# Kernel tuning notes

Measured on AMD Instinct MI355X. Metric: run time of the kernel, lower is better.

The kernel has to match this reference:

```python
import jax, jax.numpy as jnp
import numpy as np

N_NODES = 100000
N_EDGES = 1600000
IN_CH = 128
HID = 128
EMBED = 256
NUM_GRAPHS = 128


def setup_inputs() -> dict:
    key = jax.random.key(0)
    ks = jax.random.split(key, 12)
    x = jax.random.normal(ks[0], (N_NODES, IN_CH), dtype=jnp.float32)
    edge_index = jax.random.randint(ks[1], (2, N_EDGES), 0, N_NODES, dtype=jnp.int64)
    batch = jnp.sort(jax.random.randint(ks[2], (N_NODES,), 0, NUM_GRAPHS, dtype=jnp.int64))
    s = 0.05
    # conv1 MLP: Linear(in_ch,128) -> ReLU -> Linear(128,128)
    W11 = jax.random.normal(ks[3], (IN_CH, HID), dtype=jnp.float32) * s
    b11 = jnp.zeros((HID,), dtype=jnp.float32)
    W12 = jax.random.normal(ks[4], (HID, HID), dtype=jnp.float32) * s
    b12 = jnp.zeros((HID,), dtype=jnp.float32)
    # conv2 MLP: Linear(128,128) -> ReLU -> Linear(128,embed)
    W21 = jax.random.normal(ks[5], (HID, HID), dtype=jnp.float32) * s
    b21 = jnp.zeros((HID,), dtype=jnp.float32)
    W22 = jax.random.normal(ks[6], (HID, EMBED), dtype=jnp.float32) * s
    b22 = jnp.zeros((EMBED,), dtype=jnp.float32)
    gamma = jnp.ones((EMBED,), dtype=jnp.float32)
    beta = jnp.zeros((EMBED,), dtype=jnp.float32)
    return {"x": x, "edge_index": edge_index, "batch": batch,
            "W11": W11, "b11": b11, "W12": W12, "b12": b12,
            "W21": W21, "b21": b21, "W22": W22, "b22": b22,
            "gamma": gamma, "beta": beta}


def _gin_conv(x, src, dst, W_a, b_a, W_b, b_b):
    # GINConv with eps=0: MLP(x + sum_{j in N(i)} x_j)
    msgs = x[src]                                   # [E, d] gather
    agg = jax.ops.segment_sum(msgs, dst, num_segments=N_NODES)  # scatter-add
    h = x + agg
    h = jax.nn.relu(h @ W_a + b_a)
    return h @ W_b + b_b


def reference(x, edge_index, batch, W11, b11, W12, b12, W21, b21, W22, b22, gamma, beta):
    src, dst = edge_index[0], edge_index[1]
    h = jax.nn.relu(_gin_conv(x, src, dst, W11, b11, W12, b12))   # [N, 128]
    h = jax.nn.relu(_gin_conv(h, src, dst, W21, b21, W22, b22))   # [N, 256]
    # global_mean_pool over graphs
    sums = jax.ops.segment_sum(h, batch, num_segments=NUM_GRAPHS)           # [G, 256]
    counts = jax.ops.segment_sum(jnp.ones((N_NODES,), h.dtype), batch, num_segments=NUM_GRAPHS)
    pooled = sums / jnp.maximum(counts, 1.0)[:, None]
    # LayerNorm over last dim (eps=1e-5 as in torch)
    mu = jnp.mean(pooled, axis=-1, keepdims=True)
    var = jnp.var(pooled, axis=-1, keepdims=True)
    out = (pooled - mu) * jax.lax.rsqrt(var + 1e-5) * gamma + beta
    # Dropout in eval mode: identity
    return out
```

## Files before the change

kernel.cpp:

```cpp
#include <hip/hip_runtime.h>

#define GRAPHS 128
#define CHUNKC 4000

typedef _Float16 f16x8 __attribute__((ext_vector_type(8)));
typedef _Float16 f16x4 __attribute__((ext_vector_type(4)));
typedef _Float16 f16x2 __attribute__((ext_vector_type(2)));
typedef float f32x4 __attribute__((ext_vector_type(4)));

__device__ __forceinline__ void fmix_lo(float& a, int w) {
  asm("v_fma_mix_f32 %0, %1, 1.0, %0 op_sel:[0,0,0] op_sel_hi:[1,0,0]" : "+v"(a) : "v"(w));
}
__device__ __forceinline__ void fmix_hi(float& a, int w) {
  asm("v_fma_mix_f32 %0, %1, 1.0, %0 op_sel:[1,0,0] op_sel_hi:[1,0,0]" : "+v"(a) : "v"(w));
}

__global__ void k_hist(const int* __restrict__ dst, int* __restrict__ histG,
                       int e, int NB, int NW) {
  __shared__ int h[256];
  int t = threadIdx.x, w = blockIdx.x;
  h[t] = 0; __syncthreads();
  int lo = w * CHUNKC, hi = min(lo + CHUNKC, e);
  for (int i = lo + t; i < hi; i += 256) atomicAdd(&h[dst[i] >> 9], 1);
  __syncthreads();
  if (t < NB) histG[t * NW + w] = h[t];
}

__global__ void k_scanA(const int* __restrict__ in, int* __restrict__ out,
                        int* __restrict__ bsum, int N) {
  __shared__ int s[256];
  int t = threadIdx.x, b = blockIdx.x;
  int base = b * 1024 + t * 4;
  int v[4]; int tot = 0;
#pragma unroll
  for (int j = 0; j < 4; ++j) { int i = base + j; v[j] = (i < N) ? in[i] : 0; tot += v[j]; }
  s[t] = tot; __syncthreads();
  for (int o = 1; o < 256; o <<= 1) {
    int x = (t >= o) ? s[t - o] : 0;
    __syncthreads(); s[t] += x; __syncthreads();
  }
  int run = s[t] - tot;
#pragma unroll
  for (int j = 0; j < 4; ++j) { int i = base + j; if (i < N) out[i] = run; run += v[j]; }
  if (t == 255) bsum[b] = s[255];
}

__global__ void k_scanB(int* bsum, int nb, const int* __restrict__ batch,
                        int* __restrict__ starts, int n) {
  __shared__ int s[256];
  int t = threadIdx.x;
  int v = (t < nb) ? bsum[t] : 0;
  s[t] = v; __syncthreads();
  for (int o = 1; o < 256; o <<= 1) {
    int x = (t >= o) ? s[t - o] : 0;
    __syncthreads(); s[t] += x; __syncthreads();
  }
  if (t < nb) bsum[t] = s[t] - v;
  if (t <= GRAPHS) {
    int lo = 0, hi = n;
    while (lo < hi) { int mid = (lo + hi) >> 1; if (batch[mid] < t) lo = mid + 1; else hi = mid; }
    starts[t] = lo;
  }
}

__global__ void k_scanC(int* __restrict__ out, const int* __restrict__ bsum, int N) {
  int i = blockIdx.x * 256 + threadIdx.x;
  if (i < N) out[i] += bsum[i >> 10];
}

__global__ void k_part(const int* __restrict__ src, const int* __restrict__ dst,
                       const int* __restrict__ histG, const int* __restrict__ off,
                       int* __restrict__ part, int e, int NB, int NW) {
  __shared__ int hist[256], lbA[256], lbB[256], stmp[256];
  __shared__ int els[CHUNKC];
  int t = threadIdx.x, w = blockIdx.x;
  int hv = (t < NB) ? histG[t * NW + w] : 0;
  hist[t] = hv; stmp[t] = hv; __syncthreads();
  for (int o = 1; o < 256; o <<= 1) {
    int x = (t >= o) ? stmp[t - o] : 0;
    __syncthreads(); stmp[t] += x; __syncthreads();
  }
  lbA[t] = stmp[t] - hv; lbB[t] = stmp[t] - hv;
  __syncthreads();
  int lo = w * CHUNKC, hi = min(lo + CHUNKC, e);
  for (int i = lo + t; i < hi; i += 256) {
    int d = dst[i];
    int p = atomicAdd(&lbB[d >> 9], 1);
    els[p] = src[i] | ((d & 511) << 17);
  }
  __syncthreads();
  int ln = t & 63, wv = t >> 6;
  for (int b = wv; b < NB; b += 4) {
    int c = hist[b], lb = lbA[b];
    long g = off[b * NW + w];
    for (int j = ln; j < c; j += 64) part[g + j] = els[lb + j];
  }
}

__global__ void k_csrb(const int* __restrict__ part, const int* __restrict__ off,
                       int* __restrict__ ptr, int* __restrict__ csr,
                       int e, int NB, int NW, int n) {
  __shared__ int nh[512], ncur[512], stmp[256];
  int t = threadIdx.x, b = blockIdx.x;
  int s0 = off[b * NW];
  int e0 = (b + 1 < NB) ? off[(b + 1) * NW] : e;
  nh[t] = 0; nh[t + 256] = 0; __syncthreads();
  for (int i = s0 + t; i < e0; i += 256) atomicAdd(&nh[((unsigned)part[i]) >> 17], 1);
  __syncthreads();
  int v0 = nh[2 * t], v1 = nh[2 * t + 1];
  int ps = v0 + v1;
  stmp[t] = ps; __syncthreads();
  for (int o = 1; o < 256; o <<= 1) {
    int x = (t >= o) ? stmp[t - o] : 0;
    __syncthreads(); stmp[t] += x; __syncthreads();
  }
  int base = stmp[t] - ps;
  __syncthreads();
  nh[2 * t] = base;   nh[2 * t + 1] = base + v0;
  ncur[2 * t] = base; ncur[2 * t + 1] = base + v0;
  __syncthreads();
#pragma unroll
  for (int q = 0; q < 2; ++q) {
    int vv = t + q * 256;
    int node = (b << 9) + vv;
    if (node <= n) ptr[node] = s0 + nh[vv];
  }
  for (int i = s0 + t; i < e0; i += 256) {
    int u = part[i];
    int p = atomicAdd(&ncur[((unsigned)u) >> 17], 1);
    csr[s0 + p] = u & 0x1FFFF;
  }
}

__global__ void k_prep(const float* __restrict__ x, _Float16* __restrict__ P0,
                       _Float16* __restrict__ P1, int n,
                       const float* __restrict__ W11, const float* __restrict__ W12,
                       const float* __restrict__ W21, const float* __restrict__ W22,
                       f16x8* __restrict__ f11, f16x8* __restrict__ f12,
                       f16x8* __restrict__ f21, f16x8* __restrict__ f22,
                       float* __restrict__ pool, int cvtb, int wpb, int poolb) {
  int b = blockIdx.x, t = threadIdx.x;
  if (b < cvtb) {
    int i = b * 256 + t;
    if (i < n * 32) {
      float4 v = ((const float4*)x)[i];
      f16x4 h = { (_Float16)v.x, (_Float16)v.y, (_Float16)v.z, (_Float16)v.w };
      ((f16x4*)P0)[i] = h;
    }
    return;
  }
  b -= cvtb;
  if (b < wpb) {
    int id = b * 256 + t;
    const float* W; f16x8* F; int C, cid, fshift;
    if (id < 2048)       { W = W11; F = f11; C = 128; cid = id;        fshift = 3; }
    else if (id < 4096)  { W = W12; F = f12; C = 128; cid = id - 2048; fshift = 3; }
    else if (id < 6144)  { W = W21; F = f21; C = 128; cid = id - 4096; fshift = 3; }
    else if (id < 10240) { W = W22; F = f22; C = 256; cid = id - 6144; fshift = 4; }
    else return;
    int lane = cid & 63;
    int rest = cid >> 6;
    int fc = rest & ((1 << fshift) - 1);
    int kk = rest >> fshift;
    int cout = fc * 16 + (lane & 15);
    int kb = kk * 32 + (lane >> 4) * 8;
    f16x8 v;
#pragma unroll
    for (int q = 0; q < 8; ++q) v[q] = (_Float16)W[(size_t)(kb + q) * C + cout];
    F[cid] = v;
    return;
  }
  b -= wpb;
  if (b < poolb) {
    int i = b * 256 + t;
    if (i < GRAPHS * 256) pool[i] = 0.f;
    return;
  }
  if (t < 128) P0[(size_t)n * 128 + t] = (_Float16)0.f;
  else P1[(size_t)n * 128 + (t - 128)] = (_Float16)0.f;
}

__global__ void k_agg_h(const _Float16* __restrict__ in, _Float16* __restrict__ out,
                        const int* __restrict__ ptr, const int* __restrict__ csr, int n) {
  int gid = blockIdx.x * 256 + threadIdx.x;
  int node = gid >> 6, lane = gid & 63;
  if (node >= n) return;
  const f16x8* inp = (const f16x8*)in;
  int cb = lane & 15, rg = lane >> 4;
  f16x8 self = inp[(size_t)node * 16 + cb];
  float acc[8];
#pragma unroll
  for (int c = 0; c < 8; ++c) acc[c] = (rg == 0) ? (float)self[c] : 0.f;
  int s = ptr[node], deg = ptr[node + 1] - s;
  union W { f16x8 v; int i[4]; };
  for (int seg = 0; seg < deg; seg += 64) {
    int my = (seg + lane < deg) ? csr[s + seg + lane] : n;
    int segn = min(deg - seg, 64);
    for (int b2 = 0; b2 < segn; b2 += 32) {
      int jj[8]; W w[8];
#pragma unroll
      for (int u = 0; u < 8; ++u) jj[u] = __shfl(my, b2 + u * 4 + rg);
#pragma unroll
      for (int u = 0; u < 8; ++u) w[u].v = inp[(size_t)jj[u] * 16 + cb];
#pragma unroll
      for (int u = 0; u < 8; ++u)
#pragma unroll
        for (int p = 0; p < 4; ++p) {
          fmix_lo(acc[2 * p], w[u].i[p]);
          fmix_hi(acc[2 * p + 1], w[u].i[p]);
        }
    }
  }
#pragma unroll
  for (int c = 0; c < 8; ++c) {
    acc[c] += __shfl_xor(acc[c], 16);
    acc[c] += __shfl_xor(acc[c], 32);
  }
  if (rg == 0) {
    f16x8 r;
#pragma unroll
    for (int c = 0; c < 8; ++c) r[c] = (_Float16)acc[c];
    ((f16x8*)out)[(size_t)node * 16 + cb] = r;
  }
}

__device__ __forceinline__ f16x8 xpose(f32x4 aE, f32x4 aO, int rg) {
  union U2 { _Float16 h[2]; int i; };
  union U8 { int i[4]; f16x8 v; };
  U2 e01, e23, o01, o23;
  e01.h[0] = (_Float16)aE[0]; e01.h[1] = (_Float16)aE[1];
  e23.h[0] = (_Float16)aE[2]; e23.h[1] = (_Float16)aE[3];
  o01.h[0] = (_Float16)aO[0]; o01.h[1] = (_Float16)aO[1];
  o23.h[0] = (_Float16)aO[2]; o23.h[1] = (_Float16)aO[3];
  int e01x1 = __shfl_xor(e01.i, 16), e01x2 = __shfl_xor(e01.i, 32), e01x3 = __shfl_xor(e01.i, 48);
  int e23x1 = __shfl_xor(e23.i, 16), e23x2 = __shfl_xor(e23.i, 32), e23x3 = __shfl_xor(e23.i, 48);
  int o01x1 = __shfl_xor(o01.i, 16), o01x2 = __shfl_xor(o01.i, 32), o01x3 = __shfl_xor(o01.i, 48);
  int o23x1 = __shfl_xor(o23.i, 16), o23x2 = __shfl_xor(o23.i, 32), o23x3 = __shfl_xor(o23.i, 48);
  U8 r;
  r.i[0] = rg == 0 ? e01.i : rg == 1 ? e01x3 : rg == 2 ? o01x2 : o01x1;
  r.i[1] = rg == 0 ? e23.i : rg == 1 ? e23x3 : rg == 2 ? o23x2 : o23x1;
  r.i[2] = rg == 0 ? e01x1 : rg == 1 ? e01x2 : rg == 2 ? o01x3 : o01.i;
  r.i[3] = rg == 0 ? e23x1 : rg == 1 ? e23x2 : rg == 2 ? o23x3 : o23.i;
  return r.v;
}

__launch_bounds__(256, 3)
__global__ void k_mlp128(const _Float16* __restrict__ in, const f16x8* __restrict__ wfA,
                         const float* __restrict__ bA, const f16x8* __restrict__ wfB,
                         const float* __restrict__ bB, _Float16* __restrict__ out, int n) {
  __shared__ f16x8 wf[2048];
  int t = threadIdx.x;
  int r0 = blockIdx.x * 128;
  int lane = t & 63, w = t >> 6;
  int l16 = lane & 15, rg = lane >> 4;
  int rw = w * 32;
  const f16x8* inp = (const f16x8*)in;
#pragma unroll
  for (int i = 0; i < 8; ++i) wf[t + i * 256] = wfA[t + i * 256];
  int ra0 = r0 + rw + l16;      if (ra0 > n) ra0 = n;
  int ra1 = r0 + rw + 16 + l16; if (ra1 > n) ra1 = n;
  f16x8 xf[2][4];
#pragma unroll
  for (int kk = 0; kk < 4; ++kk) {
    xf[0][kk] = inp[(size_t)ra0 * 16 + kk * 4 + rg];
    xf[1][kk] = inp[(size_t)ra1 * 16 + kk * 4 + rg];
  }
  __syncthreads();
  f32x4 acc[2][8];
#pragma unroll
  for (int rs = 0; rs < 2; ++rs)
#pragma unroll
    for (int fc = 0; fc < 8; ++fc) acc[rs][fc] = (f32x4){0.f, 0.f, 0.f, 0.f};
#pragma unroll
  for (int kk = 0; kk < 4; ++kk)
#pragma unroll
    for (int fc = 0; fc < 8; ++fc) {
      f16x8 a = wf[(kk * 8 + fc) * 64 + lane];
      acc[0][fc] = __builtin_amdgcn_mfma_f32_16x16x32_f16(a, xf[0][kk], acc[0][fc], 0, 0, 0);
      acc[1][fc] = __builtin_amdgcn_mfma_f32_16x16x32_f16(a, xf[1][kk], acc[1][fc], 0, 0, 0);
    }
  f16x8 hf[2][4];
#pragma unroll
  for (int fc = 0; fc < 8; ++fc) {
    float4 bv = *(const float4*)(bA + fc * 16 + rg * 4);
#pragma unroll
    for (int rs = 0; rs < 2; ++rs) {
      acc[rs][fc][0] = fmaxf(acc[rs][fc][0] + bv.x, 0.f);
      acc[rs][fc][1] = fmaxf(acc[rs][fc][1] + bv.y, 0.f);
      acc[rs][fc][2] = fmaxf(acc[rs][fc][2] + bv.z, 0.f);
      acc[rs][fc][3] = fmaxf(acc[rs][fc][3] + bv.w, 0.f);
    }
  }
#pragma unroll
  for (int rs = 0; rs < 2; ++rs)
#pragma unroll
    for (int kk = 0; kk < 4; ++kk)
      hf[rs][kk] = xpose(acc[rs][2 * kk], acc[rs][2 * kk + 1], rg);
  __syncthreads();
#pragma unroll
  for (int i = 0; i < 8; ++i) wf[t + i * 256] = wfB[t + i * 256];
  __syncthreads();
#pragma unroll
  for (int rs = 0; rs < 2; ++rs)
#pragma unroll
    for (int fc = 0; fc < 8; ++fc) acc[rs][fc] = (f32x4){0.f, 0.f, 0.f, 0.f};
#pragma unroll
  for (int kk = 0; kk < 4; ++kk)
#pragma unroll
    for (int fc = 0; fc < 8; ++fc) {
      f16x8 b = wf[(kk * 8 + fc) * 64 + lane];
      acc[0][fc] = __builtin_amdgcn_mfma_f32_16x16x32_f16(b, hf[0][kk], acc[0][fc], 0, 0, 0);
      acc[1][fc] = __builtin_amdgcn_mfma_f32_16x16x32_f16(b, hf[1][kk], acc[1][fc], 0, 0, 0);
    }
#pragma unroll
  for (int fc = 0; fc < 8; ++fc) {
    float4 bv = *(const float4*)(bB + fc * 16 + rg * 4);
#pragma unroll
    for (int rs = 0; rs < 2; ++rs) {
      acc[rs][fc][0] = fmaxf(acc[rs][fc][0] + bv.x, 0.f);
      acc[rs][fc][1] = fmaxf(acc[rs][fc][1] + bv.y, 0.f);
      acc[rs][fc][2] = fmaxf(acc[rs][fc][2] + bv.z, 0.f);
      acc[rs][fc][3] = fmaxf(acc[rs][fc][3] + bv.w, 0.f);
    }
  }
  f16x8* outp = (f16x8*)out;
#pragma unroll
  for (int rs = 0; rs < 2; ++rs) {
    int row = r0 + rw + rs * 16 + l16;
#pragma unroll
    for (int kk = 0; kk < 4; ++kk) {
      f16x8 o = xpose(acc[rs][2 * kk], acc[rs][2 * kk + 1], rg);
      if (row < n) outp[(size_t)row * 16 + kk * 4 + rg] = o;
    }
  }
}

__launch_bounds__(256, 3)
__global__ void k_mlp_pool(const _Float16* __restrict__ in, const f16x8* __restrict__ wfA,
                           const float* __restrict__ bA, const f16x8* __restrict__ wfB,
                           const float* __restrict__ bB, const int* __restrict__ batch,
                           float* __restrict__ pool, int n) {
  __shared__ f16x8 wf[2048];
  __shared__ float pool_l[8 * 256];
  int t = threadIdx.x;
  int r0 = blockIdx.x * 128;
  int lane = t & 63, w = t >> 6;
  int l16 = lane & 15, rg = lane >> 4;
  int rw = w * 32;
  const f16x8* inp = (const f16x8*)in;
#pragma unroll
  for (int j = 0; j < 8; ++j) pool_l[j * 256 + t] = 0.f;
#pragma unroll
  for (int i = 0; i < 8; ++i) wf[t + i * 256] = wfA[t + i * 256];
  int ra0 = r0 + rw + l16;      if (ra0 > n) ra0 = n;
  int ra1 = r0 + rw + 16 + l16; if (ra1 > n) ra1 = n;
  f16x8 xf[2][4];
#pragma unroll
  for (int kk = 0; kk < 4; ++kk) {
    xf[0][kk] = inp[(size_t)ra0 * 16 + kk * 4 + rg];
    xf[1][kk] = inp[(size_t)ra1 * 16 + kk * 4 + rg];
  }
  int g0 = batch[r0];
  int rloc = rw + rg * 4;
  int g4[2][4];
#pragma unroll
  for (int fr = 0; fr < 2; ++fr)
#pragma unroll
    for (int j = 0; j < 4; ++j) {
      int row = r0 + rloc + fr * 16 + j;
      g4[fr][j] = (row < n) ? batch[row] : -1;
    }
  __syncthreads();
  f32x4 acc[2][8];
#pragma unroll
  for (int rs = 0; rs < 2; ++rs)
#pragma unroll
    for (int fc = 0; fc < 8; ++fc) acc[rs][fc] = (f32x4){0.f, 0.f, 0.f, 0.f};
#pragma unroll
  for (int kk = 0; kk < 4; ++kk)
#pragma unroll
    for (int fc = 0; fc < 8; ++fc) {
      f16x8 a = wf[(kk * 8 + fc) * 64 + lane];
      acc[0][fc] = __builtin_amdgcn_mfma_f32_16x16x32_f16(a, xf[0][kk], acc[0][fc], 0, 0, 0);
      acc[1][fc] = __builtin_amdgcn_mfma_f32_16x16x32_f16(a, xf[1][kk], acc[1][fc], 0, 0, 0);
    }
  f16x8 hf[2][4];
#pragma unroll
  for (int fc = 0; fc < 8; ++fc) {
    float4 bv = *(const float4*)(bA + fc * 16 + rg * 4);
#pragma unroll
    for (int rs = 0; rs < 2; ++rs) {
      acc[rs][fc][0] = fmaxf(acc[rs][fc][0] + bv.x, 0.f);
      acc[rs][fc][1] = fmaxf(acc[rs][fc][1] + bv.y, 0.f);
      acc[rs][fc][2] = fmaxf(acc[rs][fc][2] + bv.z, 0.f);
      acc[rs][fc][3] = fmaxf(acc[rs][fc][3] + bv.w, 0.f);
    }
  }
#pragma unroll
  for (int rs = 0; rs < 2; ++rs)
#pragma unroll
    for (int kk = 0; kk < 4; ++kk)
      hf[rs][kk] = xpose(acc[rs][2 * kk], acc[rs][2 * kk + 1], rg);
  for (int h = 0; h < 2; ++h) {
    __syncthreads();
#pragma unroll
    for (int i = 0; i < 8; ++i) {
      int id = t + i * 256;
      int lj = id & 63, fcl = (id >> 6) & 7, kk = id >> 9;
      wf[id] = wfB[(kk * 16 + h * 8 + fcl) * 64 + lj];
    }
    __syncthreads();
#pragma unroll
    for (int rs = 0; rs < 2; ++rs)
#pragma unroll
      for (int fc = 0; fc < 8; ++fc) acc[rs][fc] = (f32x4){0.f, 0.f, 0.f, 0.f};
#pragma unroll
    for (int kk = 0; kk < 4; ++kk)
#pragma unroll
      for (int fc = 0; fc < 8; ++fc) {
        f16x8 b = wf[(kk * 8 + fc) * 64 + lane];
        acc[0][fc] = __builtin_amdgcn_mfma_f32_16x16x32_f16(hf[0][kk], b, acc[0][fc], 0, 0, 0);
        acc[1][fc] = __builtin_amdgcn_mfma_f32_16x16x32_f16(hf[1][kk], b, acc[1][fc], 0, 0, 0);
      }
#pragma unroll
    for (int fc = 0; fc < 8; ++fc) {
      int col = h * 128 + fc * 16 + l16;
      float bv = bB[col];
#pragma unroll
      for (int fr = 0; fr < 2; ++fr) {
        f32x4 a = acc[fr][fc];
        float run = fmaxf(a[0] + bv, 0.f);
#pragma unroll
        for (int j = 1; j < 4; ++j) {
          float v = fmaxf(a[j] + bv, 0.f);
          if (g4[fr][j] == g4[fr][j - 1]) run += v;
          else {
            int g = g4[fr][j - 1];
            if (g >= 0) {
              int d = g - g0;
              if (d >= 0 && d < 8) atomicAdd(&pool_l[d * 256 + col], run);
              else atomicAdd(&pool[g * 256 + col], run);
            }
            run = v;
          }
        }
        int g = g4[fr][3];
        if (g >= 0) {
          int d = g - g0;
          if (d >= 0 && d < 8) atomicAdd(&pool_l[d * 256 + col], run);
          else atomicAdd(&pool[g * 256 + col], run);
        }
      }
    }
  }
  __syncthreads();
#pragma unroll
  for (int j = 0; j < 8; ++j) {
    int idx = j * 256 + t;
    int g = g0 + (idx >> 8), col = idx & 255;
    float v = pool_l[idx];
    if (g < GRAPHS && v != 0.f) atomicAdd(&pool[g * 256 + col], v);
  }
}

__global__ void k_final(const float* __restrict__ pool, const int* __restrict__ starts,
                        const float* __restrict__ gamma, const float* __restrict__ beta,
                        float* __restrict__ out) {
  __shared__ float2 red[256];
  int g = blockIdx.x, ch = threadIdx.x;
  int cnt = starts[g + 1] - starts[g];
  float p = pool[g * 256 + ch] / fmaxf((float)cnt, 1.f);
  red[ch] = make_float2(p, p * p);
  __syncthreads();
  for (int off = 128; off > 0; off >>= 1) {
    if (ch < off) { red[ch].x += red[ch + off].x; red[ch].y += red[ch + off].y; }
    __syncthreads();
  }
  float mu = red[0].x * (1.f / 256.f);
  float var = red[0].y * (1.f / 256.f) - mu * mu;
  out[g * 256 + ch] = (p - mu) * rsqrtf(var + 1e-5f) * gamma[ch] + beta[ch];
}

extern "C" void kernel_launch(void* const* d_in, const int* in_sizes, int n_in,
                              void* d_out, int out_size, void* d_ws, size_t ws_size,
                              hipStream_t stream) {
  const float* x     = (const float*)d_in[0];
  const int*   ei    = (const int*)d_in[1];
  const int*   batch = (const int*)d_in[2];
  const float* W11 = (const float*)d_in[3];  const float* b11 = (const float*)d_in[4];
  const float* W12 = (const float*)d_in[5];  const float* b12 = (const float*)d_in[6];
  const float* W21 = (const float*)d_in[7];  const float* b21 = (const float*)d_in[8];
  const float* W22 = (const float*)d_in[9];  const float* b22 = (const float*)d_in[10];
  const float* gamma = (const float*)d_in[11];
  const float* beta  = (const float*)d_in[12];
  float* out = (float*)d_out;

  int n = in_sizes[0] / 128;
  int e = in_sizes[1] / 2;
  const int* src = ei;
  const int* dstv = ei + e;

  int NB = (n + 511) >> 9;
  int NW = (e + CHUNKC - 1) / CHUNKC;
  int NS = NB * NW;

  char* ws = (char*)d_ws;
  auto alloc = [&](size_t bytes) { char* p = ws; ws += (bytes + 15) & ~(size_t)15; return p; };
  _Float16* P0 = (_Float16*)alloc((size_t)(n + 1) * 128 * 2);
  _Float16* P1 = (_Float16*)alloc((size_t)(n + 1) * 128 * 2);
  float* pool  = (float*)alloc((size_t)GRAPHS * 256 * 4);
  int* ptr     = (int*)alloc((size_t)(n + 1) * 4);
  int* csr     = (int*)alloc((size_t)e * 4);
  int* part    = (int*)alloc((size_t)e * 4);
  int* histG   = (int*)alloc((size_t)NS * 4);
  int* off     = (int*)alloc((size_t)NS * 4);
  int* bsum    = (int*)alloc(256 * 4);
  int* starts  = (int*)alloc((GRAPHS + 1) * 4);
  f16x8* f11 = (f16x8*)alloc(2048 * 16);
  f16x8* f12 = (f16x8*)alloc(2048 * 16);
  f16x8* f21 = (f16x8*)alloc(2048 * 16);
  f16x8* f22 = (f16x8*)alloc(4096 * 16);

  int cvtb = (n * 32 + 255) / 256;
  int wpb = 40;
  int poolb = (GRAPHS * 256 + 255) / 256;
  int prepb = cvtb + wpb + poolb + 1;

  int nbk = (NS + 1023) / 1024;
  k_prep <<<prepb, 256, 0, stream>>>(x, P0, P1, n, W11, W12, W21, W22,
                                     f11, f12, f21, f22, pool, cvtb, wpb, poolb);
  k_hist <<<NW, 256, 0, stream>>>(dstv, histG, e, NB, NW);
  k_scanA<<<nbk, 256, 0, stream>>>(histG, off, bsum, NS);
  k_scanB<<<1, 256, 0, stream>>>(bsum, nbk, batch, starts, n);
  k_scanC<<<(NS + 255) / 256, 256, 0, stream>>>(off, bsum, NS);
  k_part <<<NW, 256, 0, stream>>>(src, dstv, histG, off, part, e, NB, NW);
  k_csrb <<<NB, 256, 0, stream>>>(part, off, ptr, csr, e, NB, NW, n);

  int mb = (n + 127) / 128;
  int ab = (n * 64 + 255) / 256;

  k_agg_h<<<ab, 256, 0, stream>>>(P0, P1, ptr, csr, n);
  k_mlp128<<<mb, 256, 0, stream>>>(P1, f11, b11, f12, b12, P0, n);
  k_agg_h<<<ab, 256, 0, stream>>>(P0, P1, ptr, csr, n);
  k_mlp_pool<<<mb, 256, 0, stream>>>(P1, f21, b21, f22, b22, batch, pool, n);
  k_final<<<GRAPHS, 256, 0, stream>>>(pool, starts, gamma, beta, out);
}
```

Measured before the change: 282.1 us.

## Fuse histogram into prep, fold scanC into consumers, split pool MLP by column half

The edge histogram kernel is merged into the prep kernel as extra blocks. The scanC pass is removed; k_part and k_csrb now add the block-level scan offset themselves. The final MLP+pool kernel now launches twice as many blocks, each computing one 128-column half of the output, which halves the per-block shared pool buffer. The intent is to remove two launches and add parallelism to the last stage, at the cost of recomputing the first MLP layer in both halves and doing more global atomics.

```diff
diff --git a/kernel.cpp b/kernel.cpp
--- a/kernel.cpp
+++ b/kernel.cpp
@@ -15,137 +15,32 @@
   asm("v_fma_mix_f32 %0, %1, 1.0, %0 op_sel:[1,0,0] op_sel_hi:[1,0,0]" : "+v"(a) : "v"(w));
 }
 
-__global__ void k_hist(const int* __restrict__ dst, int* __restrict__ histG,
-                       int e, int NB, int NW) {
-  __shared__ int h[256];
-  int t = threadIdx.x, w = blockIdx.x;
-  h[t] = 0; __syncthreads();
-  int lo = w * CHUNKC, hi = min(lo + CHUNKC, e);
-  for (int i = lo + t; i < hi; i += 256) atomicAdd(&h[dst[i] >> 9], 1);
-  __syncthreads();
-  if (t < NB) histG[t * NW + w] = h[t];
-}
-
-__global__ void k_scanA(const int* __restrict__ in, int* __restrict__ out,
-                        int* __restrict__ bsum, int N) {
-  __shared__ int s[256];
-  int t = threadIdx.x, b = blockIdx.x;
-  int base = b * 1024 + t * 4;
-  int v[4]; int tot = 0;
-#pragma unroll
-  for (int j = 0; j < 4; ++j) { int i = base + j; v[j] = (i < N) ? in[i] : 0; tot += v[j]; }
-  s[t] = tot; __syncthreads();
-  for (int o = 1; o < 256; o <<= 1) {
-    int x = (t >= o) ? s[t - o] : 0;
-    __syncthreads(); s[t] += x; __syncthreads();
-  }
-  int run = s[t] - tot;
-#pragma unroll
-  for (int j = 0; j < 4; ++j) { int i = base + j; if (i < N) out[i] = run; run += v[j]; }
-  if (t == 255) bsum[b] = s[255];
-}
-
-__global__ void k_scanB(int* bsum, int nb, const int* __restrict__ batch,
-                        int* __restrict__ starts, int n) {
-  __shared__ int s[256];
-  int t = threadIdx.x;
-  int v = (t < nb) ? bsum[t] : 0;
-  s[t] = v; __syncthreads();
-  for (int o = 1; o < 256; o <<= 1) {
-    int x = (t >= o) ? s[t - o] : 0;
-    __syncthreads(); s[t] += x; __syncthreads();
-  }
-  if (t < nb) bsum[t] = s[t] - v;
-  if (t <= GRAPHS) {
-    int lo = 0, hi = n;
-    while (lo < hi) { int mid = (lo + hi) >> 1; if (batch[mid] < t) lo = mid + 1; else hi = mid; }
-    starts[t] = lo;
-  }
-}
-
-__global__ void k_scanC(int* __restrict__ out, const int* __restrict__ bsum, int N) {
-  int i = blockIdx.x * 256 + threadIdx.x;
-  if (i < N) out[i] += bsum[i >> 10];
-}
-
-__global__ void k_part(const int* __restrict__ src, const int* __restrict__ dst,
-                       const int* __restrict__ histG, const int* __restrict__ off,
-                       int* __restrict__ part, int e, int NB, int NW) {
-  __shared__ int hist[256], lbA[256], lbB[256], stmp[256];
-  __shared__ int els[CHUNKC];
-  int t = threadIdx.x, w = blockIdx.x;
-  int hv = (t < NB) ? histG[t * NW + w] : 0;
-  hist[t] = hv; stmp[t] = hv; __syncthreads();
-  for (int o = 1; o < 256; o <<= 1) {
-    int x = (t >= o) ? stmp[t - o] : 0;
-    __syncthreads(); stmp[t] += x; __syncthreads();
-  }
-  lbA[t] = stmp[t] - hv; lbB[t] = stmp[t] - hv;
-  __syncthreads();
-  int lo = w * CHUNKC, hi = min(lo + CHUNKC, e);
-  for (int i = lo + t; i < hi; i += 256) {
-    int d = dst[i];
-    int p = atomicAdd(&lbB[d >> 9], 1);
-    els[p] = src[i] | ((d & 511) << 17);
-  }
-  __syncthreads();
-  int ln = t & 63, wv = t >> 6;
-  for (int b = wv; b < NB; b += 4) {
-    int c = hist[b], lb = lbA[b];
-    long g = off[b * NW + w];
-    for (int j = ln; j < c; j += 64) part[g + j] = els[lb + j];
-  }
-}
-
-__global__ void k_csrb(const int* __restrict__ part, const int* __restrict__ off,
-                       int* __restrict__ ptr, int* __restrict__ csr,
-                       int e, int NB, int NW, int n) {
-  __shared__ int nh[512], ncur[512], stmp[256];
-  int t = threadIdx.x, b = blockIdx.x;
-  int s0 = off[b * NW];
-  int e0 = (b + 1 < NB) ? off[(b + 1) * NW] : e;
-  nh[t] = 0; nh[t + 256] = 0; __syncthreads();
-  for (int i = s0 + t; i < e0; i += 256) atomicAdd(&nh[((unsigned)part[i]) >> 17], 1);
-  __syncthreads();
-  int v0 = nh[2 * t], v1 = nh[2 * t + 1];
-  int ps = v0 + v1;
-  stmp[t] = ps; __syncthreads();
-  for (int o = 1; o < 256; o <<= 1) {
-    int x = (t >= o) ? stmp[t - o] : 0;
-    __syncthreads(); stmp[t] += x; __syncthreads();
-  }
-  int base = stmp[t] - ps;
-  __syncthreads();
-  nh[2 * t] = base;   nh[2 * t + 1] = base + v0;
-  ncur[2 * t] = base; ncur[2 * t + 1] = base + v0;
-  __syncthreads();
-#pragma unroll
-  for (int q = 0; q < 2; ++q) {
-    int vv = t + q * 256;
-    int node = (b << 9) + vv;
-    if (node <= n) ptr[node] = s0 + nh[vv];
-  }
-  for (int i = s0 + t; i < e0; i += 256) {
-    int u = part[i];
-    int p = atomicAdd(&ncur[((unsigned)u) >> 17], 1);
-    csr[s0 + p] = u & 0x1FFFF;
-  }
-}
-
-__global__ void k_prep(const float* __restrict__ x, _Float16* __restrict__ P0,
+__global__ void k_prep(const int* __restrict__ dst, int* __restrict__ histG,
+                       int e, int NB, int NW,
+                       const float* __restrict__ x, _Float16* __restrict__ P0,
                        _Float16* __restrict__ P1, int n,
                        const float* __restrict__ W11, const float* __restrict__ W12,
                        const float* __restrict__ W21, const float* __restrict__ W22,
                        f16x8* __restrict__ f11, f16x8* __restrict__ f12,
                        f16x8* __restrict__ f21, f16x8* __restrict__ f22,
                        float* __restrict__ pool, int cvtb, int wpb, int poolb) {
+  __shared__ int h[256];
   int b = blockIdx.x, t = threadIdx.x;
+  if (b < NW) {
+    h[t] = 0; __syncthreads();
+    int lo = b * CHUNKC, hi = min(lo + CHUNKC, e);
+    for (int i = lo + t; i < hi; i += 256) atomicAdd(&h[dst[i] >> 9], 1);
+    __syncthreads();
+    if (t < NB) histG[t * NW + b] = h[t];
+    return;
+  }
+  b -= NW;
   if (b < cvtb) {
     int i = b * 256 + t;
     if (i < n * 32) {
       float4 v = ((const float4*)x)[i];
-      f16x4 h = { (_Float16)v.x, (_Float16)v.y, (_Float16)v.z, (_Float16)v.w };
-      ((f16x4*)P0)[i] = h;
+      f16x4 hh = { (_Float16)v.x, (_Float16)v.y, (_Float16)v.z, (_Float16)v.w };
+      ((f16x4*)P0)[i] = hh;
     }
     return;
   }
@@ -178,6 +73,112 @@
   }
   if (t < 128) P0[(size_t)n * 128 + t] = (_Float16)0.f;
   else P1[(size_t)n * 128 + (t - 128)] = (_Float16)0.f;
+}
+
+__global__ void k_scanA(const int* __restrict__ in, int* __restrict__ out,
+                        int* __restrict__ bsum, int N) {
+  __shared__ int s[256];
+  int t = threadIdx.x, b = blockIdx.x;
+  int base = b * 1024 + t * 4;
+  int v[4]; int tot = 0;
+#pragma unroll
+  for (int j = 0; j < 4; ++j) { int i = base + j; v[j] = (i < N) ? in[i] : 0; tot += v[j]; }
+  s[t] = tot; __syncthreads();
+  for (int o = 1; o < 256; o <<= 1) {
+    int x = (t >= o) ? s[t - o] : 0;
+    __syncthreads(); s[t] += x; __syncthreads();
+  }
+  int run = s[t] - tot;
+#pragma unroll
+  for (int j = 0; j < 4; ++j) { int i = base + j; if (i < N) out[i] = run; run += v[j]; }
+  if (t == 255) bsum[b] = s[255];
+}
+
+__global__ void k_scanB(int* bsum, int nb, const int* __restrict__ batch,
+                        int* __restrict__ starts, int n) {
+  __shared__ int s[256];
+  int t = threadIdx.x;
+  int v = (t < nb) ? bsum[t] : 0;
+  s[t] = v; __syncthreads();
+  for (int o = 1; o < 256; o <<= 1) {
+    int x = (t >= o) ? s[t - o] : 0;
+    __syncthreads(); s[t] += x; __syncthreads();
+  }
+  if (t < nb) bsum[t] = s[t] - v;
+  if (t <= GRAPHS) {
+    int lo = 0, hi = n;
+    while (lo < hi) { int mid = (lo + hi) >> 1; if (batch[mid] < t) lo = mid + 1; else hi = mid; }
+    starts[t] = lo;
+  }
+}
+
+__global__ void k_part(const int* __restrict__ src, const int* __restrict__ dst,
+                       const int* __restrict__ histG, const int* __restrict__ off,
+                       const int* __restrict__ bsum,
+                       int* __restrict__ part, int e, int NB, int NW) {
+  __shared__ int hist[256], lbA[256], lbB[256], stmp[256];
+  __shared__ int els[CHUNKC];
+  int t = threadIdx.x, w = blockIdx.x;
+  int hv = (t < NB) ? histG[t * NW + w] : 0;
+  hist[t] = hv; stmp[t] = hv; __syncthreads();
+  for (int o = 1; o < 256; o <<= 1) {
+    int x = (t >= o) ? stmp[t - o] : 0;
+    __syncthreads(); stmp[t] += x; __syncthreads();
+  }
+  lbA[t] = stmp[t] - hv; lbB[t] = stmp[t] - hv;
+  __syncthreads();
+  int lo = w * CHUNKC, hi = min(lo + CHUNKC, e);
+  for (int i = lo + t; i < hi; i += 256) {
+    int d = dst[i];
+    int p = atomicAdd(&lbB[d >> 9], 1);
+    els[p] = src[i] | ((d & 511) << 17);
+  }
+  __syncthreads();
+  int ln = t & 63, wv = t >> 6;
+  for (int b = wv; b < NB; b += 4) {
+    int c = hist[b], lb = lbA[b];
+    int idx = b * NW + w;
+    long g = off[idx] + bsum[idx >> 10];
+    for (int j = ln; j < c; j += 64) part[g + j] = els[lb + j];
+  }
+}
+
+__global__ void k_csrb(const int* __restrict__ part, const int* __restrict__ off,
+                       const int* __restrict__ bsum,
+                       int* __restrict__ ptr, int* __restrict__ csr,
+                       int e, int NB, int NW, int n) {
+  __shared__ int nh[512], ncur[512], stmp[256];
+  int t = threadIdx.x, b = blockIdx.x;
+  int i0 = b * NW;
+  int s0 = off[i0] + bsum[i0 >> 10];
+  int e0 = e;
+  if (b + 1 < NB) { int i1 = (b + 1) * NW; e0 = off[i1] + bsum[i1 >> 10]; }
+  nh[t] = 0; nh[t + 256] = 0; __syncthreads();
+  for (int i = s0 + t; i < e0; i += 256) atomicAdd(&nh[((unsigned)part[i]) >> 17], 1);
+  __syncthreads();
+  int v0 = nh[2 * t], v1 = nh[2 * t + 1];
+  int ps = v0 + v1;
+  stmp[t] = ps; __syncthreads();
+  for (int o = 1; o < 256; o <<= 1) {
+    int x = (t >= o) ? stmp[t - o] : 0;
+    __syncthreads(); stmp[t] += x; __syncthreads();
+  }
+  int base = stmp[t] - ps;
+  __syncthreads();
+  nh[2 * t] = base;   nh[2 * t + 1] = base + v0;
+  ncur[2 * t] = base; ncur[2 * t + 1] = base + v0;
+  __syncthreads();
+#pragma unroll
+  for (int q = 0; q < 2; ++q) {
+    int vv = t + q * 256;
+    int node = (b << 9) + vv;
+    if (node <= n) ptr[node] = s0 + nh[vv];
+  }
+  for (int i = s0 + t; i < e0; i += 256) {
+    int u = part[i];
+    int p = atomicAdd(&ncur[((unsigned)u) >> 17], 1);
+    csr[s0 + p] = u & 0x1FFFF;
+  }
 }
 
 __global__ void k_agg_h(const _Float16* __restrict__ in, _Float16* __restrict__ out,
@@ -341,15 +342,16 @@
                            const float* __restrict__ bB, const int* __restrict__ batch,
                            float* __restrict__ pool, int n) {
   __shared__ f16x8 wf[2048];
-  __shared__ float pool_l[8 * 256];
+  __shared__ float pool_l[8 * 128];
   int t = threadIdx.x;
-  int r0 = blockIdx.x * 128;
+  int h = blockIdx.x & 1;
+  int r0 = (blockIdx.x >> 1) * 128;
   int lane = t & 63, w = t >> 6;
   int l16 = lane & 15, rg = lane >> 4;
   int rw = w * 32;
   const f16x8* inp = (const f16x8*)in;
 #pragma unroll
-  for (int j = 0; j < 8; ++j) pool_l[j * 256 + t] = 0.f;
+  for (int j = 0; j < 4; ++j) pool_l[j * 256 + t] = 0.f;
 #pragma unroll
   for (int i = 0; i < 8; ++i) wf[t + i * 256] = wfA[t + i * 256];
   int ra0 = r0 + rw + l16;      if (ra0 > n) ra0 = n;
@@ -401,65 +403,63 @@
 #pragma unroll
     for (int kk = 0; kk < 4; ++kk)
       hf[rs][kk] = xpose(acc[rs][2 * kk], acc[rs][2 * kk + 1], rg);
-  for (int h = 0; h < 2; ++h) {
-    __syncthreads();
-#pragma unroll
-    for (int i = 0; i < 8; ++i) {
-      int id = t + i * 256;
-      int lj = id & 63, fcl = (id >> 6) & 7, kk = id >> 9;
-      wf[id] = wfB[(kk * 16 + h * 8 + fcl) * 64 + lj];
-    }
-    __syncthreads();
-#pragma unroll
-    for (int rs = 0; rs < 2; ++rs)
-#pragma unroll
-      for (int fc = 0; fc < 8; ++fc) acc[rs][fc] = (f32x4){0.f, 0.f, 0.f, 0.f};
-#pragma unroll
-    for (int kk = 0; kk < 4; ++kk)
-#pragma unroll
-      for (int fc = 0; fc < 8; ++fc) {
-        f16x8 b = wf[(kk * 8 + fc) * 64 + lane];
-        acc[0][fc] = __builtin_amdgcn_mfma_f32_16x16x32_f16(hf[0][kk], b, acc[0][fc], 0, 0, 0);
-        acc[1][fc] = __builtin_amdgcn_mfma_f32_16x16x32_f16(hf[1][kk], b, acc[1][fc], 0, 0, 0);
-      }
+  __syncthreads();
+#pragma unroll
+  for (int i = 0; i < 8; ++i) {
+    int id = t + i * 256;
+    int lj = id & 63, fcl = (id >> 6) & 7, kk = id >> 9;
+    wf[id] = wfB[(kk * 16 + h * 8 + fcl) * 64 + lj];
+  }
+  __syncthreads();
+#pragma unroll
+  for (int rs = 0; rs < 2; ++rs)
+#pragma unroll
+    for (int fc = 0; fc < 8; ++fc) acc[rs][fc] = (f32x4){0.f, 0.f, 0.f, 0.f};
+#pragma unroll
+  for (int kk = 0; kk < 4; ++kk)
 #pragma unroll
     for (int fc = 0; fc < 8; ++fc) {
-      int col = h * 128 + fc * 16 + l16;
-      float bv = bB[col];
-#pragma unroll
-      for (int fr = 0; fr < 2; ++fr) {
-        f32x4 a = acc[fr][fc];
-        float run = fmaxf(a[0] + bv, 0.f);
-#pragma unroll
-        for (int j = 1; j < 4; ++j) {
-          float v = fmaxf(a[j] + bv, 0.f);
-          if (g4[fr][j] == g4[fr][j - 1]) run += v;
-          else {
-            int g = g4[fr][j - 1];
-            if (g >= 0) {
-              int d = g - g0;
-              if (d >= 0 && d < 8) atomicAdd(&pool_l[d * 256 + col], run);
-              else atomicAdd(&pool[g * 256 + col], run);
-            }
-            run = v;
+      f16x8 b = wf[(kk * 8 + fc) * 64 + lane];
+      acc[0][fc] = __builtin_amdgcn_mfma_f32_16x16x32_f16(hf[0][kk], b, acc[0][fc], 0, 0, 0);
+      acc[1][fc] = __builtin_amdgcn_mfma_f32_16x16x32_f16(hf[1][kk], b, acc[1][fc], 0, 0, 0);
+    }
+#pragma unroll
+  for (int fc = 0; fc < 8; ++fc) {
+    int col128 = fc * 16 + l16;
+    float bv = bB[h * 128 + col128];
+#pragma unroll
+    for (int fr = 0; fr < 2; ++fr) {
+      f32x4 a = acc[fr][fc];
+      float run = fmaxf(a[0] + bv, 0.f);
+#pragma unroll
+      for (int j = 1; j < 4; ++j) {
+        float v = fmaxf(a[j] + bv, 0.f);
+        if (g4[fr][j] == g4[fr][j - 1]) run += v;
+        else {
+          int g = g4[fr][j - 1];
+          if (g >= 0) {
+            int d = g - g0;
+            if (d >= 0 && d < 8) atomicAdd(&pool_l[d * 128 + col128], run);
+            else atomicAdd(&pool[g * 256 + h * 128 + col128], run);
           }
-        }
-        int g = g4[fr][3];
-        if (g >= 0) {
-          int d = g - g0;
-          if (d >= 0 && d < 8) atomicAdd(&pool_l[d * 256 + col], run);
-          else atomicAdd(&pool[g * 256 + col], run);
+          run = v;
         }
       }
-    }
-  }
-  __syncthreads();
-#pragma unroll
-  for (int j = 0; j < 8; ++j) {
+      int g = g4[fr][3];
+      if (g >= 0) {
+        int d = g - g0;
+        if (d >= 0 && d < 8) atomicAdd(&pool_l[d * 128 + col128], run);
+        else atomicAdd(&pool[g * 256 + h * 128 + col128], run);
+      }
+    }
+  }
+  __syncthreads();
+#pragma unroll
+  for (int j = 0; j < 4; ++j) {
     int idx = j * 256 + t;
-    int g = g0 + (idx >> 8), col = idx & 255;
+    int g = g0 + (idx >> 7), col128 = idx & 127;
     float v = pool_l[idx];
-    if (g < GRAPHS && v != 0.f) atomicAdd(&pool[g * 256 + col], v);
+    if (g < GRAPHS && v != 0.f) atomicAdd(&pool[g * 256 + h * 128 + col128], v);
   }
 }
 
@@ -524,17 +524,16 @@
   int cvtb = (n * 32 + 255) / 256;
   int wpb = 40;
   int poolb = (GRAPHS * 256 + 255) / 256;
-  int prepb = cvtb + wpb + poolb + 1;
+  int prepb = NW + cvtb + wpb + poolb + 1;
 
   int nbk = (NS + 1023) / 1024;
-  k_prep <<<prepb, 256, 0, stream>>>(x, P0, P1, n, W11, W12, W21, W22,
-                                     f11, f12, f21, f22, pool, cvtb, wpb, poolb);
-  k_hist <<<NW, 256, 0, stream>>>(dstv, histG, e, NB, NW);
+  k_prep <<<prepb, 256, 0, stream>>>(dstv, histG, e, NB, NW, x, P0, P1, n,
+                                     W11, W12, W21, W22, f11, f12, f21, f22,
+                                     pool, cvtb, wpb, poolb);
   k_scanA<<<nbk, 256, 0, stream>>>(histG, off, bsum, NS);
   k_scanB<<<1, 256, 0, stream>>>(bsum, nbk, batch, starts, n);
-  k_scanC<<<(NS + 255) / 256, 256, 0, stream>>>(off, bsum, NS);
-  k_part <<<NW, 256, 0, stream>>>(src, dstv, histG, off, part, e, NB, NW);
-  k_csrb <<<NB, 256, 0, stream>>>(part, off, ptr, csr, e, NB, NW, n);
+  k_part <<<NW, 256, 0, stream>>>(src, dstv, histG, off, bsum, part, e, NB, NW);
+  k_csrb <<<NB, 256, 0, stream>>>(part, off, bsum, ptr, csr, e, NB, NW, n);
 
   int mb = (n + 127) / 128;
   int ab = (n * 64 + 255) / 256;
@@ -542,6 +541,6 @@
   k_agg_h<<<ab, 256, 0, stream>>>(P0, P1, ptr, csr, n);
   k_mlp128<<<mb, 256, 0, stream>>>(P1, f11, b11, f12, b12, P0, n);
   k_agg_h<<<ab, 256, 0, stream>>>(P0, P1, ptr, csr, n);
-  k_mlp_pool<<<mb, 256, 0, stream>>>(P1, f21, b21, f22, b22, batch, pool, n);
+  k_mlp_pool<<<mb * 2, 256, 0, stream>>>(P1, f21, b21, f22, b22, batch, pool, n);
   k_final<<<GRAPHS, 256, 0, stream>>>(pool, starts, gamma, beta, out);
 }
```

New measurement: 276.9 us. No clear change (-1.8%).
